# Kernel optimization log

Hardware: AMD Instinct MI355X
Metric: run time of the kernel (lower is better)

## Reference

```python
import jax, jax.numpy as jnp
import numpy as np

N_USERS = 100_000
N_ITEMS = 50_000
N = N_USERS + N_ITEMS
N_LAYERS = 3
ALPHA = 0.8
D = 64
IMG_D = 4096
TXT_D = 384
N_INTER = 2_000_000  # user-item interactions; symmetric nnz = 2*N_INTER


def setup_inputs() -> dict:
    # --- build symmetric-normalized bipartite adjacency (D^-1/2 A D^-1/2) in numpy ---
    rng = np.random.default_rng(0)
    u = rng.integers(0, N_USERS, N_INTER).astype(np.int32)
    i = (rng.integers(0, N_ITEMS, N_INTER) + N_USERS).astype(np.int32)
    rows = np.concatenate([u, i])
    cols = np.concatenate([i, u])
    deg = np.bincount(rows, minlength=N).astype(np.float32)
    d_inv = np.where(deg > 0, deg ** -0.5, 0.0).astype(np.float32)
    vals = d_inv[rows] * d_inv[cols]

    key = jax.random.key(0)
    ks = jax.random.split(key, 8)
    xav_img = float(np.sqrt(6.0 / (IMG_D + D)))
    xav_txt = float(np.sqrt(6.0 / (TXT_D + D)))
    return {
        "image_feats": jax.random.normal(ks[0], (N_ITEMS, IMG_D), jnp.float32),
        "text_feats": jax.random.normal(ks[1], (N_ITEMS, TXT_D), jnp.float32),
        "image_pref": jax.random.normal(ks[2], (N_USERS, D), jnp.float32),
        "text_pref": jax.random.normal(ks[3], (N_USERS, D), jnp.float32),
        "W_img": jax.random.uniform(ks[4], (IMG_D, D), jnp.float32, -xav_img, xav_img),
        "b_img": jnp.zeros((D,), jnp.float32),
        "W_txt": jax.random.uniform(ks[5], (TXT_D, D), jnp.float32, -xav_txt, xav_txt),
        "b_txt": jnp.zeros((D,), jnp.float32),
        "adj_vals": jnp.asarray(vals),
        "adj_rows": jnp.asarray(rows),
        "adj_cols": jnp.asarray(cols),
    }


def _spmm(rows, cols, vals, x):
    # sparse COO @ dense: out[r] += vals[e] * x[cols[e]]
    return jax.ops.segment_sum(vals[:, None] * x[cols], rows, num_segments=N)


def _l2norm(x):
    # F.normalize(x, dim=1): row-wise L2 with eps clamp
    return x / jnp.clip(jnp.linalg.norm(x, axis=1, keepdims=True), 1e-12)


def reference(image_feats, text_feats, image_pref, text_pref,
              W_img, b_img, W_txt, b_txt, adj_vals, adj_rows, adj_cols):
    img = _l2norm(image_feats @ W_img + b_img)   # [n_items, D]
    txt = _l2norm(text_feats @ W_txt + b_txt)    # [n_items, D]
    ego_i = jnp.concatenate([image_pref, img], axis=0)  # [N, D]
    ego_t = jnp.concatenate([text_pref, txt], axis=0)   # [N, D]
    for _ in range(N_LAYERS):
        ego_i = _spmm(adj_rows, adj_cols, adj_vals, ego_i) + ALPHA * ego_i
        ego_t = _spmm(adj_rows, adj_cols, adj_vals, ego_t) + ALPHA * ego_t
    user_preference = jnp.concatenate([ego_i[:N_USERS], ego_t[:N_USERS]], axis=1)  # [n_users, 2D]
    items = jnp.concatenate([ego_i[N_USERS:], ego_t[N_USERS:]], axis=1)            # [n_items, 2D]
    return user_preference, items
```

## Files before the change

### kernel.cpp

```cpp
#include <hip/hip_runtime.h>
#include <hip/hip_bf16.h>

#define N_USERS 100000
#define N_ITEMS 50000
#define N_TOTAL 150000
#define NNZ     4000000
#define ALPHA_F 0.8f
#define ELL_CAP 128

#define C_COPY 512
#define C_SCAT 1024
#define G_GEMM 3125
#define NC_IMG 32
#define NC_ALL 35

typedef __attribute__((ext_vector_type(8))) short bf16x8;
typedef __attribute__((ext_vector_type(4))) float f32x4;

static __device__ __forceinline__ short f2bf(float f) {
    unsigned u = __builtin_bit_cast(unsigned, f);
    unsigned r = (u + 0x7fff + ((u >> 16) & 1)) >> 16;
    return (short)r;
}
static __device__ __forceinline__ unsigned pack_bf2(float a, float b) {
    return (unsigned)(unsigned short)f2bf(a) | ((unsigned)(unsigned short)f2bf(b) << 16);
}
static __device__ __forceinline__ float bf_lo(unsigned u) { return __uint_as_float(u << 16); }
static __device__ __forceinline__ float bf_hi(unsigned u) { return __uint_as_float(u & 0xFFFF0000u); }

static __device__ __forceinline__ void gload_lds16(const void* src, void* dst) {
    __builtin_amdgcn_global_load_lds(
        (const __attribute__((address_space(1))) unsigned*)src,
        (__attribute__((address_space(3))) unsigned*)dst, 16, 0, 0);
}


__global__ __launch_bounds__(256) void prep_kernel(const float* __restrict__ Wimg,
                                                   const float* __restrict__ Wtxt,
                                                   int* __restrict__ cnt,
                                                   char* __restrict__ WtiT,
                                                   char* __restrict__ WttT) {
    const int T0 = N_TOTAL;
    const int T1 = T0 + 4096 * 64;
    const int T2 = T1 + 384 * 64;
    int i = blockIdx.x * 256 + threadIdx.x;
    int stride = gridDim.x * 256;
    for (; i < T2; i += stride) {
        if (i < T0) {
            cnt[i] = 0;
        } else if (i < T1) {
            int idx = i - T0; int k = idx >> 6, n = idx & 63;
            int c = k >> 7, kk = k & 127;
            *(short*)(WtiT + c * 16384 + n * 256 + ((kk * 2) ^ ((n & 7) << 4)))
                = f2bf(Wimg[(size_t)k * 64 + n]);
        } else {
            int idx = i - T1; int k = idx >> 6, n = idx & 63;
            int c = k >> 7, kk = k & 127;
            *(short*)(WttT + c * 16384 + n * 256 + ((kk * 2) ^ ((n & 7) << 4)))
                = f2bf(Wtxt[(size_t)k * 64 + n]);
        }
    }
}


__global__ __launch_bounds__(256, 3) void gemm_kernel(
        const float* __restrict__ Aimg, const float* __restrict__ Atxt,
        const char* __restrict__ WtiT, const char* __restrict__ WttT,
        const float* __restrict__ bimg, const float* __restrict__ btxt,
        unsigned* __restrict__ egob_items) {
    __shared__ __align__(16) char abuf[2][8192];
    __shared__ __align__(16) char bbuf[2][16384];
    const int t = threadIdx.x;
    const int wave = t >> 6, lane = t & 63;
    const int col = lane & 15, kb = lane >> 4;
    const int row0 = blockIdx.x * 16;

    auto stage = [&](int ci, int bi) {
        const float* A; size_t rowbytes; const char* BT; int cc;
        if (ci < NC_IMG) { A = Aimg; rowbytes = 16384; BT = WtiT; cc = ci; }
        else             { A = Atxt; rowbytes = 1536;  BT = WttT; cc = ci - NC_IMG; }
        #pragma unroll
        for (int q = 0; q < 2; ++q) {
            int r = (q * 4 + wave) * 2 + (lane >> 5);
            int so = ((lane & 31) * 16) ^ ((r & 7) << 4);
            const char* src = (const char*)A + (size_t)(row0 + r) * rowbytes + cc * 512 + so;
            char* dst = abuf[bi] + (q * 4 + wave) * 1024 + lane * 16;
            gload_lds16(src, dst);
        }
        #pragma unroll
        for (int q = 0; q < 4; ++q) {
            int off = (q * 4 + wave) * 1024 + lane * 16;
            gload_lds16(BT + (size_t)cc * 16384 + off, bbuf[bi] + off);
        }
    };

    auto comp = [&](int bi, f32x4& acc) {
        const int r = col;
        const int aswz = (r & 7) << 4;
        const char* ab = abuf[bi] + r * 512;
        const int n = 16 * wave + col;
        const char* bb = bbuf[bi] + n * 256;
        const int bswz = (n & 7) << 4;
        #pragma unroll
        for (int ks = 0; ks < 4; ++ks) {
            int la = ks * 128 + kb * 32;
            float4 a0 = *(const float4*)(ab + (la ^ aswz));
            float4 a1 = *(const float4*)(ab + ((la + 16) ^ aswz));
            bf16x8 af;
            af[0]=f2bf(a0.x); af[1]=f2bf(a0.y); af[2]=f2bf(a0.z); af[3]=f2bf(a0.w);
            af[4]=f2bf(a1.x); af[5]=f2bf(a1.y); af[6]=f2bf(a1.z); af[7]=f2bf(a1.w);
            bf16x8 bf = *(const bf16x8*)(bb + ((ks * 64 + kb * 16) ^ bswz));
            acc = __builtin_amdgcn_mfma_f32_16x16x32_bf16(af, bf, acc, 0, 0, 0);
        }
    };

    f32x4 ai = {0.f,0.f,0.f,0.f}, at4 = {0.f,0.f,0.f,0.f};

    stage(0, 0);
    for (int ci = 0; ci < NC_ALL; ++ci) {
        int bi = ci & 1;
        if (ci + 1 < NC_ALL) {
            stage(ci + 1, bi ^ 1);
            asm volatile("s_waitcnt vmcnt(6)" ::: "memory");
        } else {
            asm volatile("s_waitcnt vmcnt(0)" ::: "memory");
        }
        __builtin_amdgcn_s_barrier();
        __builtin_amdgcn_sched_barrier(0);
        if (ci < NC_IMG) comp(bi, ai);
        else             comp(bi, at4);
        __builtin_amdgcn_sched_barrier(0);
        __builtin_amdgcn_s_barrier();
    }

    float bv_i = bimg[16 * wave + col];
    float bv_t = btxt[16 * wave + col];
    float ssi[4], sst[4];
    #pragma unroll
    for (int i = 0; i < 4; ++i) {
        ai[i] += bv_i; at4[i] += bv_t;
        ssi[i] = ai[i] * ai[i];
        sst[i] = at4[i] * at4[i];
    }
    #pragma unroll
    for (int off = 1; off < 16; off <<= 1) {
        #pragma unroll
        for (int i = 0; i < 4; ++i) {
            ssi[i] += __shfl_xor(ssi[i], off, 64);
            sst[i] += __shfl_xor(sst[i], off, 64);
        }
    }
    float* S = (float*)abuf;
    __syncthreads();
    if (col == 0) {
        #pragma unroll
        for (int i = 0; i < 4; ++i) {
            S[wave * 16 + kb * 4 + i]      = ssi[i];
            S[64 + wave * 16 + kb * 4 + i] = sst[i];
        }
    }
    __syncthreads();
    #pragma unroll
    for (int i = 0; i < 4; ++i) {
        int r = kb * 4 + i;
        float ti = S[r] + S[16 + r] + S[32 + r] + S[48 + r];
        float tt = S[64 + r] + S[80 + r] + S[96 + r] + S[112 + r];
        float rni = 1.0f / fmaxf(sqrtf(ti), 1e-12f);
        float rnt = 1.0f / fmaxf(sqrtf(tt), 1e-12f);
        egob_items[(size_t)(row0 + r) * 64 + 16 * wave + col] =
            pack_bf2(ai[i] * rni, at4[i] * rnt);
    }
}


__global__ __launch_bounds__(256) void scat_copy_kernel(
        const int* __restrict__ rows, const int* __restrict__ cols,
        const float* __restrict__ vals, int* __restrict__ cnt, int2* __restrict__ ell,
        const float* __restrict__ img_pref, const float* __restrict__ txt_pref,
        unsigned* __restrict__ egob) {
    int b = blockIdx.x;
    if (b < C_COPY) {
        int idx = b * 256 + threadIdx.x;
        int stride = C_COPY * 256;
        for (; idx < N_USERS * 16; idx += stride) {
            int row = idx >> 4, w4 = (idx & 15) << 2;
            float4 iv = *reinterpret_cast<const float4*>(&img_pref[(size_t)row * 64 + w4]);
            float4 tv = *reinterpret_cast<const float4*>(&txt_pref[(size_t)row * 64 + w4]);
            uint4 m;
            m.x = pack_bf2(iv.x, tv.x); m.y = pack_bf2(iv.y, tv.y);
            m.z = pack_bf2(iv.z, tv.z); m.w = pack_bf2(iv.w, tv.w);
            *reinterpret_cast<uint4*>(&egob[(size_t)row * 64 + w4]) = m;
        }
    } else {
        int i = (b - C_COPY) * 256 + threadIdx.x;
        int stride = C_SCAT * 256;
        for (; i < NNZ; i += stride) {
            int r = rows[i];
            int p = atomicAdd(&cnt[r], 1);
            if (p < ELL_CAP)
                ell[(size_t)r * ELL_CAP + p] = make_int2(cols[i], __float_as_int(vals[i]));
        }
    }
}


__global__ __launch_bounds__(256) void spmm_sort_kernel(
        const int* __restrict__ cnt, int2* __restrict__ ell,
        const unsigned* __restrict__ xb, unsigned* __restrict__ outb) {
    __shared__ __align__(16) int2 srt[4][ELL_CAP];
    int wid = threadIdx.x >> 6, lane = threadIdx.x & 63;
    int row = blockIdx.x * 4 + wid;
    bool valid = row < N_TOTAL;
    int deg = 0;
    int2* base = nullptr;
    int2 e0 = make_int2(0x7FFFFFFF, 0), e1 = e0;
    if (valid) {
        deg = min(cnt[row], ELL_CAP);
        base = ell + (size_t)row * ELL_CAP;
        if (lane < deg)      e0 = base[lane];
        if (lane + 64 < deg) e1 = base[lane + 64];
    }
    #pragma unroll
    for (int k = 2; k <= 128; k <<= 1) {
        #pragma unroll
        for (int j = 64; j >= 1; j >>= 1) {
            if (j >= k) continue;
            if (j == 64) {
                if (e0.x > e1.x) { int2 tmp = e0; e0 = e1; e1 = tmp; }
            } else {
                int2 p0, p1;
                p0.x = __shfl_xor(e0.x, j, 64); p0.y = __shfl_xor(e0.y, j, 64);
                p1.x = __shfl_xor(e1.x, j, 64); p1.y = __shfl_xor(e1.y, j, 64);
                bool up0 = ((lane & k) == 0);
                bool up1 = (((lane + 64) & k) == 0);
                bool lo0 = ((lane & j) == 0);
                bool keepmin0 = (up0 == lo0);
                bool keepmin1 = (up1 == lo0);
                if (keepmin0 ? (e0.x > p0.x) : (e0.x < p0.x)) e0 = p0;
                if (keepmin1 ? (e1.x > p1.x) : (e1.x < p1.x)) e1 = p1;
            }
        }
    }
    if (valid) {
        if (lane < deg)      base[lane]      = e0;
        if (lane + 64 < deg) base[lane + 64] = e1;
    }
    srt[wid][lane] = e0;
    srt[wid][lane + 64] = e1;
    __syncthreads();
    if (!valid) return;
    unsigned sw = xb[(size_t)row * 64 + lane];
    float2 acc;
    acc.x = ALPHA_F * bf_lo(sw);
    acc.y = ALPHA_F * bf_hi(sw);
    const int2* s = srt[wid];
    int i = 0;
    for (; i + 8 <= deg; i += 8) {
        int4 p0 = *reinterpret_cast<const int4*>(s + i);
        int4 p1 = *reinterpret_cast<const int4*>(s + i + 2);
        int4 p2 = *reinterpret_cast<const int4*>(s + i + 4);
        int4 p3 = *reinterpret_cast<const int4*>(s + i + 6);
        unsigned g0 = xb[(size_t)p0.x * 64 + lane];
        unsigned g1 = xb[(size_t)p0.z * 64 + lane];
        unsigned g2 = xb[(size_t)p1.x * 64 + lane];
        unsigned g3 = xb[(size_t)p1.z * 64 + lane];
        unsigned g4 = xb[(size_t)p2.x * 64 + lane];
        unsigned g5 = xb[(size_t)p2.z * 64 + lane];
        unsigned g6 = xb[(size_t)p3.x * 64 + lane];
        unsigned g7 = xb[(size_t)p3.z * 64 + lane];
        float v0 = __int_as_float(p0.y), v1 = __int_as_float(p0.w);
        float v2 = __int_as_float(p1.y), v3 = __int_as_float(p1.w);
        float v4 = __int_as_float(p2.y), v5 = __int_as_float(p2.w);
        float v6 = __int_as_float(p3.y), v7 = __int_as_float(p3.w);
        acc.x = fmaf(v0, bf_lo(g0), acc.x); acc.y = fmaf(v0, bf_hi(g0), acc.y);
        acc.x = fmaf(v1, bf_lo(g1), acc.x); acc.y = fmaf(v1, bf_hi(g1), acc.y);
        acc.x = fmaf(v2, bf_lo(g2), acc.x); acc.y = fmaf(v2, bf_hi(g2), acc.y);
        acc.x = fmaf(v3, bf_lo(g3), acc.x); acc.y = fmaf(v3, bf_hi(g3), acc.y);
        acc.x = fmaf(v4, bf_lo(g4), acc.x); acc.y = fmaf(v4, bf_hi(g4), acc.y);
        acc.x = fmaf(v5, bf_lo(g5), acc.x); acc.y = fmaf(v5, bf_hi(g5), acc.y);
        acc.x = fmaf(v6, bf_lo(g6), acc.x); acc.y = fmaf(v6, bf_hi(g6), acc.y);
        acc.x = fmaf(v7, bf_lo(g7), acc.x); acc.y = fmaf(v7, bf_hi(g7), acc.y);
    }
    for (; i < deg; ++i) {
        int2 c = s[i];
        float v = __int_as_float(c.y);
        unsigned g = xb[(size_t)c.x * 64 + lane];
        acc.x = fmaf(v, bf_lo(g), acc.x);
        acc.y = fmaf(v, bf_hi(g), acc.y);
    }
    outb[(size_t)row * 64 + lane] = pack_bf2(acc.x, acc.y);
}


__global__ __launch_bounds__(256) void spmm_kernel(
        const int* __restrict__ cnt, const int2* __restrict__ ell,
        const unsigned* __restrict__ xb,
        float* __restrict__ out32, unsigned* __restrict__ outb) {
    int row = blockIdx.x * 4 + (threadIdx.x >> 6);
    if (row >= N_TOTAL) return;
    int lane = threadIdx.x & 63;
    unsigned sw = xb[(size_t)row * 64 + lane];
    float2 acc;
    acc.x = ALPHA_F * bf_lo(sw);
    acc.y = ALPHA_F * bf_hi(sw);
    int deg = min(cnt[row], ELL_CAP);
    const int2* base = ell + (size_t)row * ELL_CAP;
    int i = 0;
    for (; i + 8 <= deg; i += 8) {
        int4 p0 = *reinterpret_cast<const int4*>(base + i);
        int4 p1 = *reinterpret_cast<const int4*>(base + i + 2);
        int4 p2 = *reinterpret_cast<const int4*>(base + i + 4);
        int4 p3 = *reinterpret_cast<const int4*>(base + i + 6);
        unsigned g0 = xb[(size_t)p0.x * 64 + lane];
        unsigned g1 = xb[(size_t)p0.z * 64 + lane];
        unsigned g2 = xb[(size_t)p1.x * 64 + lane];
        unsigned g3 = xb[(size_t)p1.z * 64 + lane];
        unsigned g4 = xb[(size_t)p2.x * 64 + lane];
        unsigned g5 = xb[(size_t)p2.z * 64 + lane];
        unsigned g6 = xb[(size_t)p3.x * 64 + lane];
        unsigned g7 = xb[(size_t)p3.z * 64 + lane];
        float v0 = __int_as_float(p0.y), v1 = __int_as_float(p0.w);
        float v2 = __int_as_float(p1.y), v3 = __int_as_float(p1.w);
        float v4 = __int_as_float(p2.y), v5 = __int_as_float(p2.w);
        float v6 = __int_as_float(p3.y), v7 = __int_as_float(p3.w);
        acc.x = fmaf(v0, bf_lo(g0), acc.x); acc.y = fmaf(v0, bf_hi(g0), acc.y);
        acc.x = fmaf(v1, bf_lo(g1), acc.x); acc.y = fmaf(v1, bf_hi(g1), acc.y);
        acc.x = fmaf(v2, bf_lo(g2), acc.x); acc.y = fmaf(v2, bf_hi(g2), acc.y);
        acc.x = fmaf(v3, bf_lo(g3), acc.x); acc.y = fmaf(v3, bf_hi(g3), acc.y);
        acc.x = fmaf(v4, bf_lo(g4), acc.x); acc.y = fmaf(v4, bf_hi(g4), acc.y);
        acc.x = fmaf(v5, bf_lo(g5), acc.x); acc.y = fmaf(v5, bf_hi(g5), acc.y);
        acc.x = fmaf(v6, bf_lo(g6), acc.x); acc.y = fmaf(v6, bf_hi(g6), acc.y);
        acc.x = fmaf(v7, bf_lo(g7), acc.x); acc.y = fmaf(v7, bf_hi(g7), acc.y);
    }
    for (; i < deg; ++i) {
        int2 c = base[i];
        float v = __int_as_float(c.y);
        unsigned g = xb[(size_t)c.x * 64 + lane];
        acc.x = fmaf(v, bf_lo(g), acc.x);
        acc.y = fmaf(v, bf_hi(g), acc.y);
    }
    if (out32) {
        out32[(size_t)row * 128 + lane] = acc.x;
        out32[(size_t)row * 128 + 64 + lane] = acc.y;
    }
    if (outb)
        outb[(size_t)row * 64 + lane] = pack_bf2(acc.x, acc.y);
}


extern "C" void kernel_launch(void* const* d_in, const int* in_sizes, int n_in,
                              void* d_out, int out_size, void* d_ws, size_t ws_size,
                              hipStream_t stream) {
    const float* image_feats = (const float*)d_in[0];
    const float* text_feats  = (const float*)d_in[1];
    const float* image_pref  = (const float*)d_in[2];
    const float* text_pref   = (const float*)d_in[3];
    const float* W_img       = (const float*)d_in[4];
    const float* b_img       = (const float*)d_in[5];
    const float* W_txt       = (const float*)d_in[6];
    const float* b_txt       = (const float*)d_in[7];
    const float* adj_vals    = (const float*)d_in[8];
    const int*   adj_rows    = (const int*)d_in[9];
    const int*   adj_cols    = (const int*)d_in[10];

    float* out = (float*)d_out;

    char* ws = (char*)d_ws;
    size_t off = 0;
    auto alloc = [&](size_t bytes) { char* p = ws + off; off += (bytes + 255) & ~size_t(255); return p; };
    int*      cnt   = (int*)     alloc(N_TOTAL * sizeof(int));
    int2*     ell   = (int2*)    alloc((size_t)N_TOTAL * ELL_CAP * sizeof(int2));
    unsigned* m0    = (unsigned*)alloc((size_t)N_TOTAL * 64 * sizeof(unsigned));
    unsigned* m1    = (unsigned*)alloc((size_t)N_TOTAL * 64 * sizeof(unsigned));
    char*     WtiT  = (char*)    alloc((size_t)NC_IMG * 16384);
    char*     WttT  = (char*)    alloc((size_t)3 * 16384);
    (void)ws_size; (void)out_size; (void)n_in; (void)in_sizes;

    prep_kernel<<<512, 256, 0, stream>>>(W_img, W_txt, cnt, WtiT, WttT);

    unsigned* m0_items = m0 + (size_t)N_USERS * 64;
    gemm_kernel<<<G_GEMM, 256, 0, stream>>>(
        image_feats, text_feats, WtiT, WttT, b_img, b_txt, m0_items);

    scat_copy_kernel<<<C_COPY + C_SCAT, 256, 0, stream>>>(
        adj_rows, adj_cols, adj_vals, cnt, ell, image_pref, text_pref, m0);

    const int ROW_GRID = (N_TOTAL + 3) / 4;
    spmm_sort_kernel<<<ROW_GRID, 256, 0, stream>>>(cnt, ell, m0, m1);
    spmm_kernel<<<ROW_GRID, 256, 0, stream>>>(cnt, ell, m1, nullptr, m0);
    spmm_kernel<<<ROW_GRID, 256, 0, stream>>>(cnt, ell, m0, out, nullptr);
}
```

Before: 1.025 ms.

## Fuse GEMM with edge scatter and user copy into one kernel; halve K-chunk

Merges the feature-projection GEMM and the COO-to-ELL scatter plus user-embedding copy into one launch, with block-index ranges selecting the role. The latency-bound atomic scatter can then overlap with the bandwidth-bound GEMM instead of running after it. The GEMM K-chunk is halved (64 instead of 128 per stage), which shrinks LDS to allow 6 blocks per CU, but doubles the number of pipeline iterations and barriers. The copy portion gets fewer blocks, and the scatter blocks are scheduled first, so they may compete with the GEMM for memory bandwidth.

```diff
diff --git a/kernel.cpp b/kernel.cpp
--- a/kernel.cpp
+++ b/kernel.cpp
@@ -8,11 +8,12 @@
 #define ALPHA_F 0.8f
 #define ELL_CAP 128
 
-#define C_COPY 512
-#define C_SCAT 1024
+#define G_SCAT 1024
+#define G_COPY 128
+#define G_PRE  (G_SCAT + G_COPY)
 #define G_GEMM 3125
-#define NC_IMG 32
-#define NC_ALL 35
+#define NC_IMG 64
+#define NC_ALL 70
 
 typedef __attribute__((ext_vector_type(8))) short bf16x8;
 typedef __attribute__((ext_vector_type(4))) float f32x4;
@@ -50,59 +51,90 @@
             cnt[i] = 0;
         } else if (i < T1) {
             int idx = i - T0; int k = idx >> 6, n = idx & 63;
-            int c = k >> 7, kk = k & 127;
-            *(short*)(WtiT + c * 16384 + n * 256 + ((kk * 2) ^ ((n & 7) << 4)))
+            int c = k >> 6, kk = k & 63;
+            *(short*)(WtiT + c * 8192 + n * 128 + ((kk * 2) ^ ((n & 7) << 4)))
                 = f2bf(Wimg[(size_t)k * 64 + n]);
         } else {
             int idx = i - T1; int k = idx >> 6, n = idx & 63;
-            int c = k >> 7, kk = k & 127;
-            *(short*)(WttT + c * 16384 + n * 256 + ((kk * 2) ^ ((n & 7) << 4)))
+            int c = k >> 6, kk = k & 63;
+            *(short*)(WttT + c * 8192 + n * 128 + ((kk * 2) ^ ((n & 7) << 4)))
                 = f2bf(Wtxt[(size_t)k * 64 + n]);
         }
     }
 }
 
 
-__global__ __launch_bounds__(256, 3) void gemm_kernel(
+__global__ __launch_bounds__(256, 6) void mega_kernel(
         const float* __restrict__ Aimg, const float* __restrict__ Atxt,
         const char* __restrict__ WtiT, const char* __restrict__ WttT,
         const float* __restrict__ bimg, const float* __restrict__ btxt,
-        unsigned* __restrict__ egob_items) {
-    __shared__ __align__(16) char abuf[2][8192];
-    __shared__ __align__(16) char bbuf[2][16384];
-    const int t = threadIdx.x;
-    const int wave = t >> 6, lane = t & 63;
+        unsigned* __restrict__ egob,
+        const int* __restrict__ rows, const int* __restrict__ cols,
+        const float* __restrict__ vals, int* __restrict__ cnt, int2* __restrict__ ell,
+        const float* __restrict__ img_pref, const float* __restrict__ txt_pref) {
+    __shared__ __align__(16) char abuf[2][4096];
+    __shared__ __align__(16) char bbuf[2][8192];
+    int b = blockIdx.x;
+    int t = threadIdx.x;
+    int wave = t >> 6, lane = t & 63;
+
+    if (b < G_SCAT) {
+        int i = b * 256 + t;
+        int stride = G_SCAT * 256;
+        for (; i < NNZ; i += stride) {
+            int r = rows[i];
+            int p = atomicAdd(&cnt[r], 1);
+            if (p < ELL_CAP)
+                ell[(size_t)r * ELL_CAP + p] = make_int2(cols[i], __float_as_int(vals[i]));
+        }
+        return;
+    }
+    if (b < G_PRE) {
+        int idx = (b - G_SCAT) * 256 + t;
+        int stride = G_COPY * 256;
+        for (; idx < N_USERS * 16; idx += stride) {
+            int row = idx >> 4, w4 = (idx & 15) << 2;
+            float4 iv = *reinterpret_cast<const float4*>(&img_pref[(size_t)row * 64 + w4]);
+            float4 tv = *reinterpret_cast<const float4*>(&txt_pref[(size_t)row * 64 + w4]);
+            uint4 m;
+            m.x = pack_bf2(iv.x, tv.x); m.y = pack_bf2(iv.y, tv.y);
+            m.z = pack_bf2(iv.z, tv.z); m.w = pack_bf2(iv.w, tv.w);
+            *reinterpret_cast<uint4*>(&egob[(size_t)row * 64 + w4]) = m;
+        }
+        return;
+    }
+
+    const int blk = b - G_PRE;
+    const int row0 = blk * 16;
     const int col = lane & 15, kb = lane >> 4;
-    const int row0 = blockIdx.x * 16;
 
     auto stage = [&](int ci, int bi) {
         const float* A; size_t rowbytes; const char* BT; int cc;
         if (ci < NC_IMG) { A = Aimg; rowbytes = 16384; BT = WtiT; cc = ci; }
         else             { A = Atxt; rowbytes = 1536;  BT = WttT; cc = ci - NC_IMG; }
+        {
+            int r = wave * 4 + (lane >> 4);
+            int so = ((lane & 15) * 16) ^ ((r & 7) << 4);
+            const char* src = (const char*)A + (size_t)(row0 + r) * rowbytes + cc * 256 + so;
+            char* dst = abuf[bi] + wave * 1024 + lane * 16;
+            gload_lds16(src, dst);
+        }
         #pragma unroll
         for (int q = 0; q < 2; ++q) {
-            int r = (q * 4 + wave) * 2 + (lane >> 5);
-            int so = ((lane & 31) * 16) ^ ((r & 7) << 4);
-            const char* src = (const char*)A + (size_t)(row0 + r) * rowbytes + cc * 512 + so;
-            char* dst = abuf[bi] + (q * 4 + wave) * 1024 + lane * 16;
-            gload_lds16(src, dst);
-        }
-        #pragma unroll
-        for (int q = 0; q < 4; ++q) {
             int off = (q * 4 + wave) * 1024 + lane * 16;
-            gload_lds16(BT + (size_t)cc * 16384 + off, bbuf[bi] + off);
+            gload_lds16(BT + (size_t)cc * 8192 + off, bbuf[bi] + off);
         }
     };
 
     auto comp = [&](int bi, f32x4& acc) {
         const int r = col;
         const int aswz = (r & 7) << 4;
-        const char* ab = abuf[bi] + r * 512;
+        const char* ab = abuf[bi] + r * 256;
         const int n = 16 * wave + col;
-        const char* bb = bbuf[bi] + n * 256;
+        const char* bb = bbuf[bi] + n * 128;
         const int bswz = (n & 7) << 4;
         #pragma unroll
-        for (int ks = 0; ks < 4; ++ks) {
+        for (int ks = 0; ks < 2; ++ks) {
             int la = ks * 128 + kb * 32;
             float4 a0 = *(const float4*)(ab + (la ^ aswz));
             float4 a1 = *(const float4*)(ab + ((la + 16) ^ aswz));
@@ -121,7 +153,7 @@
         int bi = ci & 1;
         if (ci + 1 < NC_ALL) {
             stage(ci + 1, bi ^ 1);
-            asm volatile("s_waitcnt vmcnt(6)" ::: "memory");
+            asm volatile("s_waitcnt vmcnt(3)" ::: "memory");
         } else {
             asm volatile("s_waitcnt vmcnt(0)" ::: "memory");
         }
@@ -160,6 +192,7 @@
         }
     }
     __syncthreads();
+    unsigned* egob_items = egob + (size_t)N_USERS * 64;
     #pragma unroll
     for (int i = 0; i < 4; ++i) {
         int r = kb * 4 + i;
@@ -169,37 +202,6 @@
         float rnt = 1.0f / fmaxf(sqrtf(tt), 1e-12f);
         egob_items[(size_t)(row0 + r) * 64 + 16 * wave + col] =
             pack_bf2(ai[i] * rni, at4[i] * rnt);
-    }
-}
-
-
-__global__ __launch_bounds__(256) void scat_copy_kernel(
-        const int* __restrict__ rows, const int* __restrict__ cols,
-        const float* __restrict__ vals, int* __restrict__ cnt, int2* __restrict__ ell,
-        const float* __restrict__ img_pref, const float* __restrict__ txt_pref,
-        unsigned* __restrict__ egob) {
-    int b = blockIdx.x;
-    if (b < C_COPY) {
-        int idx = b * 256 + threadIdx.x;
-        int stride = C_COPY * 256;
-        for (; idx < N_USERS * 16; idx += stride) {
-            int row = idx >> 4, w4 = (idx & 15) << 2;
-            float4 iv = *reinterpret_cast<const float4*>(&img_pref[(size_t)row * 64 + w4]);
-            float4 tv = *reinterpret_cast<const float4*>(&txt_pref[(size_t)row * 64 + w4]);
-            uint4 m;
-            m.x = pack_bf2(iv.x, tv.x); m.y = pack_bf2(iv.y, tv.y);
-            m.z = pack_bf2(iv.z, tv.z); m.w = pack_bf2(iv.w, tv.w);
-            *reinterpret_cast<uint4*>(&egob[(size_t)row * 64 + w4]) = m;
-        }
-    } else {
-        int i = (b - C_COPY) * 256 + threadIdx.x;
-        int stride = C_SCAT * 256;
-        for (; i < NNZ; i += stride) {
-            int r = rows[i];
-            int p = atomicAdd(&cnt[r], 1);
-            if (p < ELL_CAP)
-                ell[(size_t)r * ELL_CAP + p] = make_int2(cols[i], __float_as_int(vals[i]));
-        }
     }
 }
 
@@ -372,18 +374,15 @@
     int2*     ell   = (int2*)    alloc((size_t)N_TOTAL * ELL_CAP * sizeof(int2));
     unsigned* m0    = (unsigned*)alloc((size_t)N_TOTAL * 64 * sizeof(unsigned));
     unsigned* m1    = (unsigned*)alloc((size_t)N_TOTAL * 64 * sizeof(unsigned));
-    char*     WtiT  = (char*)    alloc((size_t)NC_IMG * 16384);
-    char*     WttT  = (char*)    alloc((size_t)3 * 16384);
+    char*     WtiT  = (char*)    alloc((size_t)NC_IMG * 8192);
+    char*     WttT  = (char*)    alloc((size_t)6 * 8192);
     (void)ws_size; (void)out_size; (void)n_in; (void)in_sizes;
 
     prep_kernel<<<512, 256, 0, stream>>>(W_img, W_txt, cnt, WtiT, WttT);
 
-    unsigned* m0_items = m0 + (size_t)N_USERS * 64;
-    gemm_kernel<<<G_GEMM, 256, 0, stream>>>(
-        image_feats, text_feats, WtiT, WttT, b_img, b_txt, m0_items);
-
-    scat_copy_kernel<<<C_COPY + C_SCAT, 256, 0, stream>>>(
-        adj_rows, adj_cols, adj_vals, cnt, ell, image_pref, text_pref, m0);
+    mega_kernel<<<G_PRE + G_GEMM, 256, 0, stream>>>(
+        image_feats, text_feats, WtiT, WttT, b_img, b_txt, m0,
+        adj_rows, adj_cols, adj_vals, cnt, ell, image_pref, text_pref);
 
     const int ROW_GRID = (N_TOTAL + 3) / 4;
     spmm_sort_kernel<<<ROW_GRID, 256, 0, stream>>>(cnt, ell, m0, m1);
```

Result: faster. 966.8 us (-5.7%).
